# Optimization experiments

Hardware: AMD Instinct MI355X
Metric: run time of the kernel (lower is better)

## Reference

```python
import jax, jax.numpy as jnp
import numpy as np

N_NODES = 100000
K = 5
C = 16
E = 3200000  # nonzeros per shift power


def setup_inputs() -> dict:
    key = jax.random.key(0)
    k1, k2, k3, k4, k5 = jax.random.split(key, 5)
    X = jax.random.normal(k1, (N_NODES, C), dtype=jnp.float32)
    rows = jax.random.randint(k2, (K, E), 0, N_NODES, dtype=jnp.int32)
    cols = jax.random.randint(k3, (K, E), 0, N_NODES, dtype=jnp.int32)
    vals = jax.random.normal(k4, (K, E), dtype=jnp.float32)
    h = jax.random.normal(k5, (C, K), dtype=jnp.float32)  # per-channel filter taps
    return {"X": X, "rows": rows, "cols": cols, "vals": vals, "h": h}


def reference(X, rows, cols, vals, h):
    # Original math: y = sum_c sum_k h[c,k] * (S_k @ X[:, c])
    #              = sum_k S_k @ (X @ h[:, k])
    N = X.shape[0]
    Kp, Ep = rows.shape
    Z = X @ h  # [N, K] combined per-tap signals
    # gather Z at source nodes for each tap: Zg[k, e] = Z[cols[k, e], k]
    Zg = Z[cols, jnp.arange(Kp, dtype=cols.dtype)[:, None]]  # [K, E]
    contrib = vals * Zg  # [K, E]
    y = jax.ops.segment_sum(contrib.reshape(-1), rows.reshape(-1), num_segments=N)
    return y  # [N]
```

## Files before the change

### kernel.cpp

```cpp
#include <hip/hip_runtime.h>
#include <hip/hip_fp16.h>

#define N_NODES 100000
#define KK 5
#define CC 16
#define EE 3200000
#define NXCC 8

#define NB 16
#define ROWS_PB 6250
#define WCAP 384
#define WPAD 385
#define BPB 64
#define CHUNK 5120
#define NCHUNK 3125
#define BLK_PER_K 625
#define SGRID 256

typedef unsigned int uint2v __attribute__((ext_vector_type(2)));

__device__ __forceinline__ int xcc_id() {
    int x;
    asm volatile("s_getreg_b32 %0, hwreg(HW_REG_XCC_ID)" : "=s"(x));
    return x & (NXCC - 1);
}

__global__ void compute_z_kernel(const float* __restrict__ X,
                                 const float* __restrict__ h,
                                 float* __restrict__ Zt,
                                 __half* __restrict__ Zh) {
    int n = blockIdx.x * blockDim.x + threadIdx.x;
    if (n >= N_NODES) return;
    const float4* Xr = (const float4*)(X + (size_t)n * CC);
    float4 x0 = Xr[0], x1 = Xr[1], x2 = Xr[2], x3 = Xr[3];
    float xv[CC] = {x0.x, x0.y, x0.z, x0.w, x1.x, x1.y, x1.z, x1.w,
                    x2.x, x2.y, x2.z, x2.w, x3.x, x3.y, x3.z, x3.w};
#pragma unroll
    for (int k = 0; k < KK; ++k) {
        float acc = 0.0f;
#pragma unroll
        for (int c = 0; c < CC; ++c) acc += xv[c] * h[c * KK + k];
        Zt[k * N_NODES + n] = acc;
        Zh[k * N_NODES + n] = __float2half_rn(acc);
    }
}

template<int SN>
__global__ __launch_bounds__(512, 2)
void scatter_lds_kernel(const int* __restrict__ rows,
                        const int* __restrict__ cols,
                        const float* __restrict__ vals,
                        const __half* __restrict__ Zh,
                        unsigned int* __restrict__ binned,
                        int* __restrict__ counts,
                        float* __restrict__ spill) {
    extern __shared__ char dynlds[];
    __half*       zsl = (__half*)dynlds;
    unsigned int* buf = (unsigned int*)(dynlds + (size_t)SN * 2);
    __shared__ int lcnt[NB];
    int tid = threadIdx.x;
    int bid = blockIdx.x;
    int w0 = (int)(((long long)NCHUNK * bid) / SGRID);
    int w1 = (int)(((long long)NCHUNK * (bid + 1)) / SGRID);

    int klast = -1;
    for (int w = w0; w < w1; ++w) {
        int k = w / BLK_PER_K;
        const __half* Zk_h = Zh + (size_t)k * N_NODES;
        if (SN > 0 && k != klast) {
            __syncthreads();
            const float4* zsrc = (const float4*)Zk_h;
            float4*       zdst = (float4*)dynlds;
#pragma unroll
            for (int i = 0; i < SN / 4096; ++i)
                zdst[tid + i * 512] = zsrc[tid + i * 512];
            klast = k;
            __syncthreads();
        }
        if (tid < NB) lcnt[tid] = 0;
        __syncthreads();

        int cbase = w * CHUNK;
        int e0 = cbase + tid * 4;
        int e1 = cbase + 2048 + tid * 4;
        int e2 = cbase + 4096 + tid * 2;
        int4   r0 = *(const int4*)(rows + e0);
        int4   c0 = *(const int4*)(cols + e0);
        float4 v0 = *(const float4*)(vals + e0);
        int4   r1 = *(const int4*)(rows + e1);
        int4   c1 = *(const int4*)(cols + e1);
        float4 v1 = *(const float4*)(vals + e1);
        int2   r2 = *(const int2*)(rows + e2);
        int2   c2 = *(const int2*)(cols + e2);
        float2 v2 = *(const float2*)(vals + e2);

        int   cc[10] = {c0.x, c0.y, c0.z, c0.w, c1.x, c1.y, c1.z, c1.w, c2.x, c2.y};
        int   rr[10] = {r0.x, r0.y, r0.z, r0.w, r1.x, r1.y, r1.z, r1.w, r2.x, r2.y};
        float vv[10] = {v0.x, v0.y, v0.z, v0.w, v1.x, v1.y, v1.z, v1.w, v2.x, v2.y};

        float z[10];
#pragma unroll
        for (int i = 0; i < 10; ++i) {
            unsigned c = (unsigned)cc[i];
            __half hz;
            if (SN > 0 && c < (unsigned)SN) hz = zsl[c];
            else                            hz = Zk_h[c];
            z[i] = __half2float(hz);
        }

        int pos[10];
#pragma unroll
        for (int i = 0; i < 10; ++i) {
            int b = rr[i] / ROWS_PB;
            pos[i] = atomicAdd(&lcnt[b], 1);
        }

#pragma unroll
        for (int i = 0; i < 10; ++i) {
            int b = rr[i] / ROWS_PB;
            float cb = vv[i] * z[i];
            int p = pos[i];
            if (p < WCAP) {
                unsigned int packed =
                    ((unsigned)(rr[i] - b * ROWS_PB) << 16) |
                    (unsigned)__half_as_ushort(__float2half_rn(cb));
                buf[b * WPAD + p] = packed;
            } else {
                unsafeAtomicAdd(&spill[rr[i]], cb);
            }
        }
        __syncthreads();

        unsigned int* wbase = binned + (size_t)w * WCAP;
#pragma unroll 1
        for (int b = 0; b < NB; ++b) {
            int cnt = min(lcnt[b], WCAP);
            if (tid < cnt)
                wbase[(size_t)b * ((size_t)NCHUNK * WCAP) + tid] = buf[b * WPAD + tid];
        }
        if (tid < NB) counts[w * NB + tid] = min(lcnt[tid], WCAP);
        __syncthreads();
    }
}

__global__ __launch_bounds__(512, 2)
void accum_kernel(const unsigned int* __restrict__ binned,
                  const int* __restrict__ counts,
                  float* __restrict__ partials) {
    __shared__ float acc[ROWS_PB];
    __shared__ int cnts[56];
    int b = blockIdx.x / BPB;
    int s = blockIdx.x % BPB;
    int tid = threadIdx.x;
    int wlo = (NCHUNK * s) / BPB;
    int whi = (NCHUNK * (s + 1)) / BPB;
    for (int i = tid; i < ROWS_PB; i += 512) acc[i] = 0.0f;
    if (tid < whi - wlo) cnts[tid] = counts[(wlo + tid) * NB + b];
    __syncthreads();

    const unsigned int* bbase = binned + (size_t)b * ((size_t)NCHUNK * WCAP);
    int t    = tid & 255;
    int half = tid >> 8;
    for (int w0 = wlo; w0 < whi; w0 += 16) {
        uint2v e[8];
        int ok0[8], ok1[8];
#pragma unroll
        for (int j = 0; j < 8; ++j) {
            int w = w0 + 2 * j + half;
            int cnt = (w < whi) ? cnts[w - wlo] : 0;
            ok0[j] = 2 * t < cnt;
            ok1[j] = 2 * t + 1 < cnt;
            const uint2v* src = (const uint2v*)(bbase + (size_t)w * WCAP);
            uint2v ez = {0u, 0u};
            e[j] = ok0[j] ? src[t] : ez;
        }
#pragma unroll
        for (int j = 0; j < 8; ++j) {
            if (ok0[j])
                atomicAdd(&acc[e[j][0] >> 16],
                          __half2float(__ushort_as_half((unsigned short)(e[j][0] & 0xFFFFu))));
            if (ok1[j])
                atomicAdd(&acc[e[j][1] >> 16],
                          __half2float(__ushort_as_half((unsigned short)(e[j][1] & 0xFFFFu))));
        }
    }
    __syncthreads();
    float* dst = partials + (size_t)blockIdx.x * ROWS_PB;
    for (int i = tid; i < ROWS_PB; i += 512) dst[i] = acc[i];
}

__global__ void reduce_kernel(const float* __restrict__ partials,
                              const float* __restrict__ spill,
                              float* __restrict__ y) {
    int n = blockIdx.x * blockDim.x + threadIdx.x;
    if (n >= N_NODES) return;
    int b = n / ROWS_PB, loc = n - b * ROWS_PB;
    const float* p = partials + (size_t)(b * BPB) * ROWS_PB + loc;
    float acc = spill[n];
#pragma unroll 8
    for (int s = 0; s < BPB; ++s) acc += p[(size_t)s * ROWS_PB];
    y[n] = acc;
}

__global__ void edge_kernel_atomic(const int* __restrict__ rows,
                                   const int* __restrict__ cols,
                                   const float* __restrict__ vals,
                                   const float* __restrict__ Zt,
                                   float* __restrict__ yrep) {
    int t = blockIdx.x * blockDim.x + threadIdx.x;
    int base = t * 4;
    if (base >= KK * EE) return;
    int k = base / EE;
    const float* Zk = Zt + (size_t)k * N_NODES;
    float* y = yrep + (size_t)xcc_id() * N_NODES;
    int4 r = *(const int4*)(rows + base);
    int4 c = *(const int4*)(cols + base);
    float4 v = *(const float4*)(vals + base);
    unsafeAtomicAdd(&y[r.x], v.x * Zk[c.x]);
    unsafeAtomicAdd(&y[r.y], v.y * Zk[c.y]);
    unsafeAtomicAdd(&y[r.z], v.z * Zk[c.z]);
    unsafeAtomicAdd(&y[r.w], v.w * Zk[c.w]);
}

__global__ void reduce8_kernel(const float* __restrict__ yrep, float* __restrict__ y) {
    int n = blockIdx.x * blockDim.x + threadIdx.x;
    if (n >= N_NODES) return;
    float acc = 0.0f;
#pragma unroll
    for (int r = 0; r < NXCC; ++r) acc += yrep[(size_t)r * N_NODES + n];
    y[n] = acc;
}

extern "C" void kernel_launch(void* const* d_in, const int* in_sizes, int n_in,
                              void* d_out, int out_size, void* d_ws, size_t ws_size,
                              hipStream_t stream) {
    const float* X    = (const float*)d_in[0];
    const int*   rows = (const int*)  d_in[1];
    const int*   cols = (const int*)  d_in[2];
    const float* vals = (const float*)d_in[3];
    const float* h    = (const float*)d_in[4];
    float* y = (float*)d_out;

    char* ws = (char*)d_ws;
    float*  Zt = (float*)ws;
    size_t zh_off      = 2000000;
    size_t counts_off  = 3000000;
    size_t spill_off   = 3200000;
    size_t binned_off  = 3600000;
    size_t binned_sz   = (size_t)NCHUNK * NB * WCAP * 4;
    size_t partial_off = binned_off + binned_sz;
    size_t partial_sz  = (size_t)NB * BPB * ROWS_PB * 4;
    size_t need = partial_off + partial_sz;
    __half* Zh = (__half*)(ws + zh_off);

    {
        int threads = 256;
        int blocks  = (N_NODES + threads - 1) / threads;
        compute_z_kernel<<<blocks, threads, 0, stream>>>(X, h, Zt, Zh);
    }

    if (ws_size >= need) {
        int*          counts   = (int*)(ws + counts_off);
        float*        spill    = (float*)(ws + spill_off);
        unsigned int* binned   = (unsigned int*)(ws + binned_off);
        float*        partials = (float*)(ws + partial_off);
        hipMemsetAsync(spill, 0, 400000, stream);

        static int g_sn = -1;
        const size_t stag = (size_t)NB * WPAD * 4;
        if (g_sn < 0) {
            g_sn = 0;
            int nb = 0;
            hipFuncSetAttribute((const void*)scatter_lds_kernel<65536>,
                                hipFuncAttributeMaxDynamicSharedMemorySize,
                                (int)(65536 * 2 + stag));
            if (hipOccupancyMaxActiveBlocksPerMultiprocessor(
                    &nb, scatter_lds_kernel<65536>, 512, 65536 * 2 + stag) == hipSuccess
                && nb >= 1) g_sn = 65536;
            if (g_sn == 0) {
                nb = 0;
                hipFuncSetAttribute((const void*)scatter_lds_kernel<49152>,
                                    hipFuncAttributeMaxDynamicSharedMemorySize,
                                    (int)(49152 * 2 + stag));
                if (hipOccupancyMaxActiveBlocksPerMultiprocessor(
                        &nb, scatter_lds_kernel<49152>, 512, 49152 * 2 + stag) == hipSuccess
                    && nb >= 1) g_sn = 49152;
            }
            if (g_sn == 0) {
                nb = 0;
                hipFuncSetAttribute((const void*)scatter_lds_kernel<32768>,
                                    hipFuncAttributeMaxDynamicSharedMemorySize,
                                    (int)(32768 * 2 + stag));
                if (hipOccupancyMaxActiveBlocksPerMultiprocessor(
                        &nb, scatter_lds_kernel<32768>, 512, 32768 * 2 + stag) == hipSuccess
                    && nb >= 1) g_sn = 32768;
            }
        }
        size_t dyn = (size_t)g_sn * 2 + stag;
        switch (g_sn) {
        case 65536:
            scatter_lds_kernel<65536><<<SGRID, 512, dyn, stream>>>(
                rows, cols, vals, Zh, binned, counts, spill);
            break;
        case 49152:
            scatter_lds_kernel<49152><<<SGRID, 512, dyn, stream>>>(
                rows, cols, vals, Zh, binned, counts, spill);
            break;
        case 32768:
            scatter_lds_kernel<32768><<<SGRID, 512, dyn, stream>>>(
                rows, cols, vals, Zh, binned, counts, spill);
            break;
        default:
            scatter_lds_kernel<0><<<SGRID, 512, dyn, stream>>>(
                rows, cols, vals, Zh, binned, counts, spill);
            break;
        }

        accum_kernel<<<NB * BPB, 512, 0, stream>>>(binned, counts, partials);
        {
            int threads = 256;
            int blocks  = (N_NODES + threads - 1) / threads;
            reduce_kernel<<<blocks, threads, 0, stream>>>(partials, spill, y);
        }
    } else {
        float* yrep = (float*)(ws + spill_off);
        hipMemsetAsync(yrep, 0, (size_t)NXCC * N_NODES * sizeof(float), stream);
        {
            int threads = 256;
            int blocks = ((KK * EE) / 4 + threads - 1) / threads;
            edge_kernel_atomic<<<blocks, threads, 0, stream>>>(rows, cols, vals, Zt, yrep);
        }
        {
            int threads = 256;
            int blocks  = (N_NODES + threads - 1) / threads;
            reduce8_kernel<<<blocks, threads, 0, stream>>>(yrep, y);
        }
    }
}
```

Measured before the change: 346.5 us.

## Compact binned entries via global per-bin cursors instead of fixed-capacity slots

The scatter kernel now claims a contiguous range in each bin through a global atomic cursor and writes entries densely. Before, each entry went into a fixed WCAP-sized slot per chunk, and a counts array recorded how many were valid. The accum kernel then streams the compact per-bin array with plain coalesced loads and no per-chunk count checks, and it uses 32 sub-blocks per bin instead of 64, which halves the partials the reduce kernel has to sum. The aim is to cut wasted memory footprint and the cost of padded, divergent reads. In exchange the scatter adds 16 global atomics per chunk and makes the output order nondeterministic, with an overflow fallback into spill atomics.

```diff
diff --git a/kernel.cpp b/kernel.cpp
--- a/kernel.cpp
+++ b/kernel.cpp
@@ -11,13 +11,12 @@
 #define ROWS_PB 6250
 #define WCAP 384
 #define WPAD 385
-#define BPB 64
+#define BPB2 32
 #define CHUNK 5120
 #define NCHUNK 3125
 #define BLK_PER_K 625
 #define SGRID 256
-
-typedef unsigned int uint2v __attribute__((ext_vector_type(2)));
+#define BSTRIDE 1081344
 
 __device__ __forceinline__ int xcc_id() {
     int x;
@@ -51,13 +50,14 @@
                         const int* __restrict__ cols,
                         const float* __restrict__ vals,
                         const __half* __restrict__ Zh,
-                        unsigned int* __restrict__ binned,
-                        int* __restrict__ counts,
+                        unsigned int* __restrict__ dense,
+                        int* __restrict__ gcursor,
                         float* __restrict__ spill) {
     extern __shared__ char dynlds[];
     __half*       zsl = (__half*)dynlds;
     unsigned int* buf = (unsigned int*)(dynlds + (size_t)SN * 2);
     __shared__ int lcnt[NB];
+    __shared__ int gbase[NB];
     int tid = threadIdx.x;
     int bid = blockIdx.x;
     int w0 = (int)(((long long)NCHUNK * bid) / SGRID);
@@ -131,62 +131,62 @@
         }
         __syncthreads();
 
-        unsigned int* wbase = binned + (size_t)w * WCAP;
+        if (tid < NB) {
+            int cnt = min(lcnt[tid], WCAP);
+            gbase[tid] = atomicAdd(&gcursor[tid], cnt);
+        }
+        __syncthreads();
+
 #pragma unroll 1
         for (int b = 0; b < NB; ++b) {
-            int cnt = min(lcnt[b], WCAP);
-            if (tid < cnt)
-                wbase[(size_t)b * ((size_t)NCHUNK * WCAP) + tid] = buf[b * WPAD + tid];
-        }
-        if (tid < NB) counts[w * NB + tid] = min(lcnt[tid], WCAP);
+            int cnt  = min(lcnt[b], WCAP);
+            int base = gbase[b];
+            int lim  = min(cnt, max(0, BSTRIDE - base));
+            unsigned int* dst = dense + (size_t)b * BSTRIDE + base;
+            if (tid < lim) dst[tid] = buf[b * WPAD + tid];
+            for (int i = lim + tid; i < cnt; i += 512) {
+                unsigned int ev = buf[b * WPAD + i];
+                unsafeAtomicAdd(&spill[b * ROWS_PB + (int)(ev >> 16)],
+                                __half2float(__ushort_as_half((unsigned short)(ev & 0xFFFFu))));
+            }
+        }
         __syncthreads();
     }
 }
 
 __global__ __launch_bounds__(512, 2)
-void accum_kernel(const unsigned int* __restrict__ binned,
-                  const int* __restrict__ counts,
+void accum_kernel(const unsigned int* __restrict__ dense,
+                  const int* __restrict__ gcursor,
                   float* __restrict__ partials) {
     __shared__ float acc[ROWS_PB];
-    __shared__ int cnts[56];
-    int b = blockIdx.x / BPB;
-    int s = blockIdx.x % BPB;
+    int b = blockIdx.x >> 5;
+    int s = blockIdx.x & 31;
     int tid = threadIdx.x;
-    int wlo = (NCHUNK * s) / BPB;
-    int whi = (NCHUNK * (s + 1)) / BPB;
+    int cnt = min(gcursor[b], BSTRIDE);
+    int lo = (int)((long long)cnt * s / BPB2);
+    int hi = (int)((long long)cnt * (s + 1) / BPB2);
     for (int i = tid; i < ROWS_PB; i += 512) acc[i] = 0.0f;
-    if (tid < whi - wlo) cnts[tid] = counts[(wlo + tid) * NB + b];
     __syncthreads();
 
-    const unsigned int* bbase = binned + (size_t)b * ((size_t)NCHUNK * WCAP);
-    int t    = tid & 255;
-    int half = tid >> 8;
-    for (int w0 = wlo; w0 < whi; w0 += 16) {
-        uint2v e[8];
-        int ok0[8], ok1[8];
-#pragma unroll
-        for (int j = 0; j < 8; ++j) {
-            int w = w0 + 2 * j + half;
-            int cnt = (w < whi) ? cnts[w - wlo] : 0;
-            ok0[j] = 2 * t < cnt;
-            ok1[j] = 2 * t + 1 < cnt;
-            const uint2v* src = (const uint2v*)(bbase + (size_t)w * WCAP);
-            uint2v ez = {0u, 0u};
-            e[j] = ok0[j] ? src[t] : ez;
-        }
-#pragma unroll
-        for (int j = 0; j < 8; ++j) {
-            if (ok0[j])
-                atomicAdd(&acc[e[j][0] >> 16],
-                          __half2float(__ushort_as_half((unsigned short)(e[j][0] & 0xFFFFu))));
-            if (ok1[j])
-                atomicAdd(&acc[e[j][1] >> 16],
-                          __half2float(__ushort_as_half((unsigned short)(e[j][1] & 0xFFFFu))));
-        }
+    const unsigned int* src = dense + (size_t)b * BSTRIDE;
+    int i = lo + tid;
+    for (; i + 512 * 7 < hi; i += 512 * 8) {
+        unsigned int e[8];
+#pragma unroll
+        for (int j = 0; j < 8; ++j) e[j] = src[i + 512 * j];
+#pragma unroll
+        for (int j = 0; j < 8; ++j)
+            atomicAdd(&acc[e[j] >> 16],
+                      __half2float(__ushort_as_half((unsigned short)(e[j] & 0xFFFFu))));
+    }
+    for (; i < hi; i += 512) {
+        unsigned int e = src[i];
+        atomicAdd(&acc[e >> 16],
+                  __half2float(__ushort_as_half((unsigned short)(e & 0xFFFFu))));
     }
     __syncthreads();
     float* dst = partials + (size_t)blockIdx.x * ROWS_PB;
-    for (int i = tid; i < ROWS_PB; i += 512) dst[i] = acc[i];
+    for (int i2 = tid; i2 < ROWS_PB; i2 += 512) dst[i2] = acc[i2];
 }
 
 __global__ void reduce_kernel(const float* __restrict__ partials,
@@ -195,10 +195,10 @@
     int n = blockIdx.x * blockDim.x + threadIdx.x;
     if (n >= N_NODES) return;
     int b = n / ROWS_PB, loc = n - b * ROWS_PB;
-    const float* p = partials + (size_t)(b * BPB) * ROWS_PB + loc;
+    const float* p = partials + (size_t)(b * BPB2) * ROWS_PB + loc;
     float acc = spill[n];
 #pragma unroll 8
-    for (int s = 0; s < BPB; ++s) acc += p[(size_t)s * ROWS_PB];
+    for (int s = 0; s < BPB2; ++s) acc += p[(size_t)s * ROWS_PB];
     y[n] = acc;
 }
 
@@ -244,12 +244,12 @@
     char* ws = (char*)d_ws;
     float*  Zt = (float*)ws;
     size_t zh_off      = 2000000;
-    size_t counts_off  = 3000000;
-    size_t spill_off   = 3200000;
-    size_t binned_off  = 3600000;
-    size_t binned_sz   = (size_t)NCHUNK * NB * WCAP * 4;
-    size_t partial_off = binned_off + binned_sz;
-    size_t partial_sz  = (size_t)NB * BPB * ROWS_PB * 4;
+    size_t cursor_off  = 3000000;
+    size_t spill_off   = 3000256;
+    size_t dense_off   = 3400256;
+    size_t dense_sz    = (size_t)NB * BSTRIDE * 4;
+    size_t partial_off = dense_off + dense_sz;
+    size_t partial_sz  = (size_t)NB * BPB2 * ROWS_PB * 4;
     size_t need = partial_off + partial_sz;
     __half* Zh = (__half*)(ws + zh_off);
 
@@ -260,11 +260,11 @@
     }
 
     if (ws_size >= need) {
-        int*          counts   = (int*)(ws + counts_off);
+        int*          gcursor  = (int*)(ws + cursor_off);
         float*        spill    = (float*)(ws + spill_off);
-        unsigned int* binned   = (unsigned int*)(ws + binned_off);
+        unsigned int* dense    = (unsigned int*)(ws + dense_off);
         float*        partials = (float*)(ws + partial_off);
-        hipMemsetAsync(spill, 0, 400000, stream);
+        hipMemsetAsync(ws + cursor_off, 0, 256 + 400000, stream);
 
         static int g_sn = -1;
         const size_t stag = (size_t)NB * WPAD * 4;
@@ -300,23 +300,23 @@
         switch (g_sn) {
         case 65536:
             scatter_lds_kernel<65536><<<SGRID, 512, dyn, stream>>>(
-                rows, cols, vals, Zh, binned, counts, spill);
+                rows, cols, vals, Zh, dense, gcursor, spill);
             break;
         case 49152:
             scatter_lds_kernel<49152><<<SGRID, 512, dyn, stream>>>(
-                rows, cols, vals, Zh, binned, counts, spill);
+                rows, cols, vals, Zh, dense, gcursor, spill);
             break;
         case 32768:
             scatter_lds_kernel<32768><<<SGRID, 512, dyn, stream>>>(
-                rows, cols, vals, Zh, binned, counts, spill);
+                rows, cols, vals, Zh, dense, gcursor, spill);
             break;
         default:
             scatter_lds_kernel<0><<<SGRID, 512, dyn, stream>>>(
-                rows, cols, vals, Zh, binned, counts, spill);
+                rows, cols, vals, Zh, dense, gcursor, spill);
             break;
         }
 
-        accum_kernel<<<NB * BPB, 512, 0, stream>>>(binned, counts, partials);
+        accum_kernel<<<NB * BPB2, 512, 0, stream>>>(dense, gcursor, partials);
         {
             int threads = 256;
             int blocks  = (N_NODES + threads - 1) / threads;
```

Measured after the change: 352.6 us. No clear change (+1.8%).

## Fuse scatter and accumulate phases with a grid barrier, drop partials buffer

Applied to the files above, without the earlier changes.

Scatter and accumulation are merged into one persistent kernel of 256 blocks separated by a software grid barrier. The accumulate phase now runs 16 slices per bin and adds its LDS totals straight into y with atomics, which removes the partials buffer and the reduce kernel. The z kernel also zeroes spill and y and resets the barrier counter, which replaces the memset launch. The cost is less parallelism in accumulation, one block per CU in the fused kernel, and a deadlock risk if the 256 blocks are not all resident at once.

```diff
diff --git a/kernel.cpp b/kernel.cpp
--- a/kernel.cpp
+++ b/kernel.cpp
@@ -11,11 +11,14 @@
 #define ROWS_PB 6250
 #define WCAP 384
 #define WPAD 385
-#define BPB 64
+#define SLICES 16
 #define CHUNK 5120
 #define NCHUNK 3125
 #define BLK_PER_K 625
 #define SGRID 256
+#define SN_MAIN 65536
+#define STAG ((size_t)NB * WPAD * 4)
+#define ACCUM_LDS (ROWS_PB * 4 + 200 * 4)
 
 typedef unsigned int uint2v __attribute__((ext_vector_type(2)));
 
@@ -25,13 +28,16 @@
     return x & (NXCC - 1);
 }
 
-__global__ void compute_z_kernel(const float* __restrict__ X,
-                                 const float* __restrict__ h,
-                                 float* __restrict__ Zt,
-                                 __half* __restrict__ Zh) {
-    int n = blockIdx.x * blockDim.x + threadIdx.x;
-    if (n >= N_NODES) return;
-    const float4* Xr = (const float4*)(X + (size_t)n * CC);
+__global__ void z_kernel(const float* __restrict__ X,
+                         const float* __restrict__ h,
+                         __half* __restrict__ Zh,
+                         float* __restrict__ spill,
+                         float* __restrict__ y,
+                         unsigned int* __restrict__ barrier_ctr) {
+    int gtid = blockIdx.x * blockDim.x + threadIdx.x;
+    if (gtid == 0) *barrier_ctr = 0;
+    if (gtid >= N_NODES) return;
+    const float4* Xr = (const float4*)(X + (size_t)gtid * CC);
     float4 x0 = Xr[0], x1 = Xr[1], x2 = Xr[2], x3 = Xr[3];
     float xv[CC] = {x0.x, x0.y, x0.z, x0.w, x1.x, x1.y, x1.z, x1.w,
                     x2.x, x2.y, x2.z, x2.w, x3.x, x3.y, x3.z, x3.w};
@@ -40,31 +46,41 @@
         float acc = 0.0f;
 #pragma unroll
         for (int c = 0; c < CC; ++c) acc += xv[c] * h[c * KK + k];
-        Zt[k * N_NODES + n] = acc;
-        Zh[k * N_NODES + n] = __float2half_rn(acc);
-    }
+        Zh[k * N_NODES + gtid] = __float2half_rn(acc);
+    }
+    spill[gtid] = 0.0f;
+    y[gtid]     = 0.0f;
+}
+
+__device__ __forceinline__ void grid_barrier(unsigned int* ctr, int tid) {
+    __syncthreads();
+    if (tid == 0) {
+        __threadfence();
+        __hip_atomic_fetch_add(ctr, 1u, __ATOMIC_ACQ_REL, __HIP_MEMORY_SCOPE_AGENT);
+        while (__hip_atomic_load(ctr, __ATOMIC_ACQUIRE, __HIP_MEMORY_SCOPE_AGENT)
+               < (unsigned)SGRID)
+            __builtin_amdgcn_s_sleep(32);
+        __threadfence();
+    }
+    __syncthreads();
 }
 
 template<int SN>
-__global__ __launch_bounds__(512, 2)
-void scatter_lds_kernel(const int* __restrict__ rows,
-                        const int* __restrict__ cols,
-                        const float* __restrict__ vals,
-                        const __half* __restrict__ Zh,
-                        unsigned int* __restrict__ binned,
-                        int* __restrict__ counts,
-                        float* __restrict__ spill) {
-    extern __shared__ char dynlds[];
+__device__ __forceinline__ void scatter_phase(const int* __restrict__ rows,
+                                              const int* __restrict__ cols,
+                                              const float* __restrict__ vals,
+                                              const __half* Zh,
+                                              unsigned int* binned,
+                                              int* counts, float* spill,
+                                              char* dynlds, int bid, int tid) {
+    __shared__ int lcnt[NB];
     __half*       zsl = (__half*)dynlds;
     unsigned int* buf = (unsigned int*)(dynlds + (size_t)SN * 2);
-    __shared__ int lcnt[NB];
-    int tid = threadIdx.x;
-    int bid = blockIdx.x;
-    int w0 = (int)(((long long)NCHUNK * bid) / SGRID);
-    int w1 = (int)(((long long)NCHUNK * (bid + 1)) / SGRID);
+    int w0b = (int)(((long long)NCHUNK * bid) / SGRID);
+    int w1b = (int)(((long long)NCHUNK * (bid + 1)) / SGRID);
 
     int klast = -1;
-    for (int w = w0; w < w1; ++w) {
+    for (int w = w0b; w < w1b; ++w) {
         int k = w / BLK_PER_K;
         const __half* Zk_h = Zh + (size_t)k * N_NODES;
         if (SN > 0 && k != klast) {
@@ -94,14 +110,14 @@
         int2   c2 = *(const int2*)(cols + e2);
         float2 v2 = *(const float2*)(vals + e2);
 
-        int   cc[10] = {c0.x, c0.y, c0.z, c0.w, c1.x, c1.y, c1.z, c1.w, c2.x, c2.y};
-        int   rr[10] = {r0.x, r0.y, r0.z, r0.w, r1.x, r1.y, r1.z, r1.w, r2.x, r2.y};
-        float vv[10] = {v0.x, v0.y, v0.z, v0.w, v1.x, v1.y, v1.z, v1.w, v2.x, v2.y};
+        int   cix[10] = {c0.x, c0.y, c0.z, c0.w, c1.x, c1.y, c1.z, c1.w, c2.x, c2.y};
+        int   rr[10]  = {r0.x, r0.y, r0.z, r0.w, r1.x, r1.y, r1.z, r1.w, r2.x, r2.y};
+        float vv[10]  = {v0.x, v0.y, v0.z, v0.w, v1.x, v1.y, v1.z, v1.w, v2.x, v2.y};
 
         float z[10];
 #pragma unroll
         for (int i = 0; i < 10; ++i) {
-            unsigned c = (unsigned)cc[i];
+            unsigned c = (unsigned)cix[i];
             __half hz;
             if (SN > 0 && c < (unsigned)SN) hz = zsl[c];
             else                            hz = Zk_h[c];
@@ -143,24 +159,23 @@
     }
 }
 
-__global__ __launch_bounds__(512, 2)
-void accum_kernel(const unsigned int* __restrict__ binned,
-                  const int* __restrict__ counts,
-                  float* __restrict__ partials) {
-    __shared__ float acc[ROWS_PB];
-    __shared__ int cnts[56];
-    int b = blockIdx.x / BPB;
-    int s = blockIdx.x % BPB;
-    int tid = threadIdx.x;
-    int wlo = (NCHUNK * s) / BPB;
-    int whi = (NCHUNK * (s + 1)) / BPB;
+__device__ __forceinline__ void accum_phase(const unsigned int* binned,
+                                            const int* counts,
+                                            const float* spill, float* y,
+                                            char* dynlds, int bid, int tid) {
+    float* acc  = (float*)dynlds;
+    int*   cnts = (int*)(dynlds + ROWS_PB * 4);
+    int b = bid >> 4;
+    int s = bid & (SLICES - 1);
+    int wlo = (NCHUNK * s) / SLICES;
+    int whi = (NCHUNK * (s + 1)) / SLICES;
+    int nw  = whi - wlo;
     for (int i = tid; i < ROWS_PB; i += 512) acc[i] = 0.0f;
-    if (tid < whi - wlo) cnts[tid] = counts[(wlo + tid) * NB + b];
+    for (int i = tid; i < nw; i += 512) cnts[i] = counts[(wlo + i) * NB + b];
     __syncthreads();
 
     const unsigned int* bbase = binned + (size_t)b * ((size_t)NCHUNK * WCAP);
-    int t    = tid & 255;
-    int half = tid >> 8;
+    int t = tid & 255, half = tid >> 8;
     for (int w0 = wlo; w0 < whi; w0 += 16) {
         uint2v e[8];
         int ok0[8], ok1[8];
@@ -185,41 +200,45 @@
         }
     }
     __syncthreads();
-    float* dst = partials + (size_t)blockIdx.x * ROWS_PB;
-    for (int i = tid; i < ROWS_PB; i += 512) dst[i] = acc[i];
-}
-
-__global__ void reduce_kernel(const float* __restrict__ partials,
-                              const float* __restrict__ spill,
-                              float* __restrict__ y) {
-    int n = blockIdx.x * blockDim.x + threadIdx.x;
-    if (n >= N_NODES) return;
-    int b = n / ROWS_PB, loc = n - b * ROWS_PB;
-    const float* p = partials + (size_t)(b * BPB) * ROWS_PB + loc;
-    float acc = spill[n];
-#pragma unroll 8
-    for (int s = 0; s < BPB; ++s) acc += p[(size_t)s * ROWS_PB];
-    y[n] = acc;
-}
-
-__global__ void edge_kernel_atomic(const int* __restrict__ rows,
+    int nbase = b * ROWS_PB;
+    if (s == 0)
+        for (int i = tid; i < ROWS_PB; i += 512) acc[i] += spill[nbase + i];
+    for (int i = tid; i < ROWS_PB; i += 512)
+        unsafeAtomicAdd(&y[nbase + i], acc[i]);
+}
+
+template<int SN>
+__global__ __launch_bounds__(512, 1)
+void fused_sa_kernel(const int* __restrict__ rows, const int* __restrict__ cols,
+                     const float* __restrict__ vals, const __half* __restrict__ Zh,
+                     unsigned int* __restrict__ binned, int* __restrict__ counts,
+                     float* __restrict__ spill, float* __restrict__ y,
+                     unsigned int* __restrict__ barrier_ctr) {
+    extern __shared__ char dynlds[];
+    int tid = threadIdx.x, bid = blockIdx.x;
+    scatter_phase<SN>(rows, cols, vals, Zh, binned, counts, spill, dynlds, bid, tid);
+    grid_barrier(barrier_ctr, tid);
+    accum_phase(binned, counts, spill, y, dynlds, bid, tid);
+}
+
+__global__ void edge_atomic_kernel(const int* __restrict__ rows,
                                    const int* __restrict__ cols,
                                    const float* __restrict__ vals,
-                                   const float* __restrict__ Zt,
+                                   const __half* __restrict__ Zh,
                                    float* __restrict__ yrep) {
     int t = blockIdx.x * blockDim.x + threadIdx.x;
     int base = t * 4;
     if (base >= KK * EE) return;
     int k = base / EE;
-    const float* Zk = Zt + (size_t)k * N_NODES;
-    float* y = yrep + (size_t)xcc_id() * N_NODES;
+    const __half* Zk = Zh + (size_t)k * N_NODES;
+    float* yr = yrep + (size_t)xcc_id() * N_NODES;
     int4 r = *(const int4*)(rows + base);
     int4 c = *(const int4*)(cols + base);
     float4 v = *(const float4*)(vals + base);
-    unsafeAtomicAdd(&y[r.x], v.x * Zk[c.x]);
-    unsafeAtomicAdd(&y[r.y], v.y * Zk[c.y]);
-    unsafeAtomicAdd(&y[r.z], v.z * Zk[c.z]);
-    unsafeAtomicAdd(&y[r.w], v.w * Zk[c.w]);
+    unsafeAtomicAdd(&yr[r.x], v.x * __half2float(Zk[c.x]));
+    unsafeAtomicAdd(&yr[r.y], v.y * __half2float(Zk[c.y]));
+    unsafeAtomicAdd(&yr[r.z], v.z * __half2float(Zk[c.z]));
+    unsafeAtomicAdd(&yr[r.w], v.w * __half2float(Zk[c.w]));
 }
 
 __global__ void reduce8_kernel(const float* __restrict__ yrep, float* __restrict__ y) {
@@ -242,93 +261,48 @@
     float* y = (float*)d_out;
 
     char* ws = (char*)d_ws;
-    float*  Zt = (float*)ws;
-    size_t zh_off      = 2000000;
-    size_t counts_off  = 3000000;
-    size_t spill_off   = 3200000;
-    size_t binned_off  = 3600000;
-    size_t binned_sz   = (size_t)NCHUNK * NB * WCAP * 4;
-    size_t partial_off = binned_off + binned_sz;
-    size_t partial_sz  = (size_t)NB * BPB * ROWS_PB * 4;
-    size_t need = partial_off + partial_sz;
-    __half* Zh = (__half*)(ws + zh_off);
-
-    {
-        int threads = 256;
-        int blocks  = (N_NODES + threads - 1) / threads;
-        compute_z_kernel<<<blocks, threads, 0, stream>>>(X, h, Zt, Zh);
-    }
+    __half*       Zh     = (__half*)ws;
+    int*          counts = (int*)(ws + 1000000);
+    float*        spill  = (float*)(ws + 1200000);
+    unsigned int* bar    = (unsigned int*)(ws + 1600000);
+    unsigned int* binned = (unsigned int*)(ws + 1600064);
+    size_t need = 1600064 + (size_t)NCHUNK * NB * WCAP * 4;
 
     if (ws_size >= need) {
-        int*          counts   = (int*)(ws + counts_off);
-        float*        spill    = (float*)(ws + spill_off);
-        unsigned int* binned   = (unsigned int*)(ws + binned_off);
-        float*        partials = (float*)(ws + partial_off);
-        hipMemsetAsync(spill, 0, 400000, stream);
-
         static int g_sn = -1;
-        const size_t stag = (size_t)NB * WPAD * 4;
+        static size_t g_dyn = 0;
         if (g_sn < 0) {
             g_sn = 0;
+            g_dyn = (STAG > (size_t)ACCUM_LDS) ? STAG : (size_t)ACCUM_LDS;
+            size_t dynM = (size_t)SN_MAIN * 2 + STAG;
+            hipFuncSetAttribute((const void*)fused_sa_kernel<SN_MAIN>,
+                                hipFuncAttributeMaxDynamicSharedMemorySize, (int)dynM);
             int nb = 0;
-            hipFuncSetAttribute((const void*)scatter_lds_kernel<65536>,
-                                hipFuncAttributeMaxDynamicSharedMemorySize,
-                                (int)(65536 * 2 + stag));
             if (hipOccupancyMaxActiveBlocksPerMultiprocessor(
-                    &nb, scatter_lds_kernel<65536>, 512, 65536 * 2 + stag) == hipSuccess
-                && nb >= 1) g_sn = 65536;
-            if (g_sn == 0) {
-                nb = 0;
-                hipFuncSetAttribute((const void*)scatter_lds_kernel<49152>,
-                                    hipFuncAttributeMaxDynamicSharedMemorySize,
-                                    (int)(49152 * 2 + stag));
-                if (hipOccupancyMaxActiveBlocksPerMultiprocessor(
-                        &nb, scatter_lds_kernel<49152>, 512, 49152 * 2 + stag) == hipSuccess
-                    && nb >= 1) g_sn = 49152;
+                    &nb, fused_sa_kernel<SN_MAIN>, 512, dynM) == hipSuccess && nb >= 1) {
+                g_sn = SN_MAIN;
+                g_dyn = dynM;
             }
-            if (g_sn == 0) {
-                nb = 0;
-                hipFuncSetAttribute((const void*)scatter_lds_kernel<32768>,
-                                    hipFuncAttributeMaxDynamicSharedMemorySize,
-                                    (int)(32768 * 2 + stag));
-                if (hipOccupancyMaxActiveBlocksPerMultiprocessor(
-                        &nb, scatter_lds_kernel<32768>, 512, 32768 * 2 + stag) == hipSuccess
-                    && nb >= 1) g_sn = 32768;
-            }
-        }
-        size_t dyn = (size_t)g_sn * 2 + stag;
-        switch (g_sn) {
-        case 65536:
-            scatter_lds_kernel<65536><<<SGRID, 512, dyn, stream>>>(
-                rows, cols, vals, Zh, binned, counts, spill);
-            break;
-        case 49152:
-            scatter_lds_kernel<49152><<<SGRID, 512, dyn, stream>>>(
-                rows, cols, vals, Zh, binned, counts, spill);
-            break;
-        case 32768:
-            scatter_lds_kernel<32768><<<SGRID, 512, dyn, stream>>>(
-                rows, cols, vals, Zh, binned, counts, spill);
-            break;
-        default:
-            scatter_lds_kernel<0><<<SGRID, 512, dyn, stream>>>(
-                rows, cols, vals, Zh, binned, counts, spill);
-            break;
-        }
-
-        accum_kernel<<<NB * BPB, 512, 0, stream>>>(binned, counts, partials);
-        {
-            int threads = 256;
-            int blocks  = (N_NODES + threads - 1) / threads;
-            reduce_kernel<<<blocks, threads, 0, stream>>>(partials, spill, y);
-        }
+        }
+
+        z_kernel<<<(N_NODES + 511) / 512, 512, 0, stream>>>(X, h, Zh, spill, y, bar);
+
+        if (g_sn == SN_MAIN)
+            fused_sa_kernel<SN_MAIN><<<SGRID, 512, g_dyn, stream>>>(
+                rows, cols, vals, Zh, binned, counts, spill, y, bar);
+        else
+            fused_sa_kernel<0><<<SGRID, 512, g_dyn, stream>>>(
+                rows, cols, vals, Zh, binned, counts, spill, y, bar);
     } else {
-        float* yrep = (float*)(ws + spill_off);
+        float* spillF = (float*)(ws + 1000000);
+        float* yrep   = (float*)(ws + 1400000);
+        unsigned int* barF = (unsigned int*)(ws + 1000000 + 399936);
+        z_kernel<<<(N_NODES + 511) / 512, 512, 0, stream>>>(X, h, Zh, spillF, y, barF);
         hipMemsetAsync(yrep, 0, (size_t)NXCC * N_NODES * sizeof(float), stream);
         {
             int threads = 256;
             int blocks = ((KK * EE) / 4 + threads - 1) / threads;
-            edge_kernel_atomic<<<blocks, threads, 0, stream>>>(rows, cols, vals, Zt, yrep);
+            edge_atomic_kernel<<<blocks, threads, 0, stream>>>(rows, cols, vals, Zh, yrep);
         }
         {
             int threads = 256;
```

Measured after the change: 383.7 us. 10.7% more time.
